# Kernel optimization log

Measured on AMD Instinct MI355X. Metric: run time of the kernel, lower is better.

Reference implementation:

```python
import jax, jax.numpy as jnp
import numpy as np

N = 120000
G = 64  # voxel grid side
HID = 128
INP = 320
CIN = HID + INP  # 448
K = 27


def _build_neighbor_map(rng):
    # unique occupied voxel cells
    cells = rng.choice(G ** 3, size=N, replace=False)
    xs = cells // (G * G)
    ys = (cells // G) % G
    zs = cells % G
    order = np.argsort(cells)
    sk = cells[order]
    offs = np.array([(dx, dy, dz) for dx in (-1, 0, 1) for dy in (-1, 0, 1) for dz in (-1, 0, 1)], dtype=np.int64)
    nx = xs[:, None] + offs[None, :, 0]
    ny = ys[:, None] + offs[None, :, 1]
    nz = zs[:, None] + offs[None, :, 2]
    valid = (nx >= 0) & (nx < G) & (ny >= 0) & (ny < G) & (nz >= 0) & (nz < G)
    nkey = (nx * G + ny) * G + nz
    pos = np.clip(np.searchsorted(sk, nkey), 0, N - 1)
    found = valid & (sk[pos] == nkey)
    return np.where(found, order[pos], -1).astype(np.int32)  # (N, 27)


def setup_inputs() -> dict:
    key = jax.random.key(0)
    ks = jax.random.split(key, 12)
    rng = np.random.default_rng(0)
    nbr = jnp.asarray(_build_neighbor_map(rng))
    s_conv = 1.0 / np.sqrt(K * CIN)
    s_lin = 1.0 / np.sqrt(CIN)
    return {
        "h": jax.random.normal(ks[0], (N, HID), jnp.float32),
        "x": jax.random.normal(ks[1], (N, INP), jnp.float32),
        "nbr": nbr,
        "Wz": jax.random.normal(ks[2], (K, CIN, HID), jnp.float32) * s_conv,
        "Wz_pt": jax.random.normal(ks[3], (CIN, HID), jnp.float32) * s_lin,
        "bz": jnp.zeros((HID,), jnp.float32),
        "Wr": jax.random.normal(ks[4], (K, CIN, HID), jnp.float32) * s_conv,
        "Wr_pt": jax.random.normal(ks[5], (CIN, HID), jnp.float32) * s_lin,
        "br": jnp.zeros((HID,), jnp.float32),
        "Wq": jax.random.normal(ks[6], (K, CIN, HID), jnp.float32) * s_conv,
        "Wq_pt": jax.random.normal(ks[7], (CIN, HID), jnp.float32) * s_lin,
        "bq": jnp.zeros((HID,), jnp.float32),
    }


def _sconv3d(F, nbr, W, W_pt, b_pt):
    # sparse 3x3x3 conv (gather + matmul accumulate over 27 offsets, no conv bias)
    # followed by voxel_to_point (identity here) + point_transforms linear.
    mask = (nbr >= 0)
    idx = jnp.where(mask, nbr, 0)
    out = F @ W_pt + b_pt  # point transform branch
    for k in range(K):  # fixed small kernel-offset loop
        g = F[idx[:, k]] * mask[:, k:k + 1].astype(F.dtype)  # (N, CIN)
        out = out + g @ W[k]
    return out


def reference(h, x, nbr, Wz, Wz_pt, bz, Wr, Wr_pt, br, Wq, Wq_pt, bq):
    hx = jnp.concatenate([h, x], axis=1)  # (N, 448)
    z = jax.nn.sigmoid(_sconv3d(hx, nbr, Wz, Wz_pt, bz))
    r = jax.nn.sigmoid(_sconv3d(hx, nbr, Wr, Wr_pt, br))
    rx = jnp.concatenate([r * h, x], axis=1)
    q = jnp.tanh(_sconv3d(rx, nbr, Wq, Wq_pt, bq))
    return (1.0 - z) * h + z * q
```

## Files before the change

kernel.cpp:

```cpp
#include <hip/hip_runtime.h>

#define NPTS   120000
#define NOFF   28
#define CHUNKS 7

typedef __bf16 bf16;
typedef __bf16 bf16x8 __attribute__((ext_vector_type(8)));
typedef float  f32x4  __attribute__((ext_vector_type(4)));

__global__ void wprep1(const float* __restrict__ Wz, const float* __restrict__ Wzp,
                       const float* __restrict__ Wr, const float* __restrict__ Wrp,
                       bf16* __restrict__ WB1)
{
    int bid  = blockIdx.x;
    int koff = bid / 56;
    int rem  = bid % 56;
    int ch   = rem / 8;
    int kseg = rem % 8;
    int n    = threadIdx.x;
    int cinb = ch * 64 + kseg * 8;
    bf16x8 v;
    if (n < 128) {
        int col = n;
        #pragma unroll
        for (int j = 0; j < 8; ++j) {
            int cin = cinb + j;
            float w = (koff < 27) ? Wz[((long)koff * 448 + cin) * 128 + col]
                                  : Wzp[(long)cin * 128 + col];
            v[j] = (bf16)w;
        }
    } else {
        int col = n - 128;
        #pragma unroll
        for (int j = 0; j < 8; ++j) {
            int cin = cinb + j;
            float w = (koff < 27) ? Wr[((long)koff * 448 + cin) * 128 + col]
                                  : Wrp[(long)cin * 128 + col];
            v[j] = (bf16)w;
        }
    }
    *(bf16x8*)(WB1 + ((long)bid * 256 + n) * 8) = v;
}

__global__ void wprep2(const float* __restrict__ Wq, const float* __restrict__ Wqp,
                       bf16* __restrict__ WB2)
{
    int bid  = blockIdx.x;
    int koff = bid / 56;
    int rem  = bid % 56;
    int ch   = rem / 8;
    int kseg = rem % 8;
    int n    = threadIdx.x;
    int cinb = ch * 64 + kseg * 8;
    bf16x8 v;
    #pragma unroll
    for (int j = 0; j < 8; ++j) {
        int cin = cinb + j;
        float w = (koff < 27) ? Wq[((long)koff * 448 + cin) * 128 + n]
                              : Wqp[(long)cin * 128 + n];
        v[j] = (bf16)w;
    }
    *(bf16x8*)(WB2 + ((long)bid * 128 + n) * 8) = v;
}

__global__ void fprep(const float* __restrict__ h, const float* __restrict__ x,
                      bf16* __restrict__ F1, bf16* __restrict__ F2)
{
    long i = (long)blockIdx.x * blockDim.x + threadIdx.x;
    if (i >= (long)NPTS * 448) return;
    int p = (int)(i / 448);
    int c = (int)(i % 448);
    float v = (c < 128) ? h[(long)p * 128 + c] : x[(long)p * 320 + (c - 128)];
    F1[i] = (bf16)v;
    if (c >= 128) F2[i] = (bf16)v;
}

template<int NCOLS, int GATE>
__global__ __launch_bounds__(NCOLS * 2)
void gconv(const bf16* __restrict__ F, const int* __restrict__ nbr,
           const bf16* __restrict__ WB, const float* __restrict__ b0,
           const float* __restrict__ b1, const float* __restrict__ hbuf,
           float* __restrict__ zbuf, bf16* __restrict__ f2,
           float* __restrict__ out, const bf16* __restrict__ zrow)
{
    constexpr int THREADS = NCOLS * 2;
    constexpr int AP = 1024 / THREADS;
    constexpr int BP = (NCOLS * 8) / THREADS;

    __shared__ __align__(16) bf16 lA[8 * 128 * 8];
    __shared__ __align__(16) bf16 lB[8 * NCOLS * 8];
    __shared__ int lidx[128];

    const int t    = threadIdx.x;
    const int lane = t & 63;
    const int w    = t >> 6;
    const int m0   = (w & 1) * 64;
    const int n0   = (w >> 1) * 64;
    const int base = blockIdx.x * 128;
    const int ar   = t & 127;
    const int aks0 = t >> 7;

    f32x4 acc[4][4];
    #pragma unroll
    for (int i = 0; i < 4; ++i)
        #pragma unroll
        for (int j = 0; j < 4; ++j)
            acc[i][j] = {0.f, 0.f, 0.f, 0.f};

    const bf16x8* lAv = (const bf16x8*)lA;
    const bf16x8* lBv = (const bf16x8*)lB;

    for (int koff = 0; koff < NOFF; ++koff) {
        __syncthreads();
        if (t < 128) {
            int p = base + t;
            int idx = -1;
            if (p < NPTS) idx = (koff == 27) ? p : nbr[(long)p * 27 + koff];
            lidx[t] = idx;
        }
        __syncthreads();
        const int myidx = lidx[ar];
        const bf16* arow = (myidx >= 0) ? (F + (long)myidx * 448) : zrow;

        for (int ch = 0; ch < CHUNKS; ++ch) {
            #pragma unroll
            for (int p = 0; p < AP; ++p) {
                int kseg = aks0 + p * (THREADS / 128);
                __builtin_amdgcn_global_load_lds(
                    (void*)(arow + ch * 64 + kseg * 8),
                    (void*)(lA + ((long)t + (long)p * THREADS) * 8),
                    16, 0, 0);
            }
            const bf16* bsrc = WB + (long)(koff * CHUNKS + ch) * (NCOLS * 64);
            #pragma unroll
            for (int p = 0; p < BP; ++p) {
                __builtin_amdgcn_global_load_lds(
                    (void*)(bsrc + ((long)t + (long)p * THREADS) * 8),
                    (void*)(lB + ((long)t + (long)p * THREADS) * 8),
                    16, 0, 0);
            }
            __syncthreads();
            #pragma unroll
            for (int kk = 0; kk < 2; ++kk) {
                const int aseg = kk * 4 + (lane >> 4);
                bf16x8 af[4], bfr[4];
                #pragma unroll
                for (int mi = 0; mi < 4; ++mi)
                    af[mi] = lAv[aseg * 128 + m0 + mi * 16 + (lane & 15)];
                #pragma unroll
                for (int ni = 0; ni < 4; ++ni)
                    bfr[ni] = lBv[aseg * NCOLS + n0 + ni * 16 + (lane & 15)];
                #pragma unroll
                for (int mi = 0; mi < 4; ++mi)
                    #pragma unroll
                    for (int ni = 0; ni < 4; ++ni)
                        acc[mi][ni] = __builtin_amdgcn_mfma_f32_16x16x32_bf16(
                            af[mi], bfr[ni], acc[mi][ni], 0, 0, 0);
            }
            __syncthreads();
        }
    }

    const int quad = lane >> 4;
    const int lc   = lane & 15;
    #pragma unroll
    for (int mi = 0; mi < 4; ++mi) {
        int rb = m0 + mi * 16 + quad * 4;
        #pragma unroll
        for (int ni = 0; ni < 4; ++ni) {
            int c = n0 + ni * 16 + lc;
            f32x4 v = acc[mi][ni];
            #pragma unroll
            for (int rg = 0; rg < 4; ++rg) {
                int p = base + rb + rg;
                if (p < NPTS) {
                    float pre = v[rg];
                    if constexpr (GATE == 1) {
                        if (c < 128) {
                            float z = 1.f / (1.f + __expf(-(pre + b0[c])));
                            zbuf[(long)p * 128 + c] = z;
                        } else {
                            int cc = c - 128;
                            float r = 1.f / (1.f + __expf(-(pre + b1[cc])));
                            f2[(long)p * 448 + cc] = (bf16)(r * hbuf[(long)p * 128 + cc]);
                        }
                    } else {
                        float q  = tanhf(pre + b0[c]);
                        float z  = zbuf[(long)p * 128 + c];
                        float hv = hbuf[(long)p * 128 + c];
                        out[(long)p * 128 + c] = (1.f - z) * hv + z * q;
                    }
                }
            }
        }
    }
}

extern "C" void kernel_launch(void* const* d_in, const int* in_sizes, int n_in,
                              void* d_out, int out_size, void* d_ws, size_t ws_size,
                              hipStream_t stream)
{
    const float* h   = (const float*)d_in[0];
    const float* x   = (const float*)d_in[1];
    const int*   nbr = (const int*)d_in[2];
    const float* Wz  = (const float*)d_in[3];
    const float* Wzp = (const float*)d_in[4];
    const float* bz  = (const float*)d_in[5];
    const float* Wr  = (const float*)d_in[6];
    const float* Wrp = (const float*)d_in[7];
    const float* br  = (const float*)d_in[8];
    const float* Wq  = (const float*)d_in[9];
    const float* Wqp = (const float*)d_in[10];
    const float* bq  = (const float*)d_in[11];
    float* out = (float*)d_out;

    char* ws = (char*)d_ws;
    bf16* WB1 = (bf16*)ws;  ws += (size_t)1568 * 256 * 8 * 2;
    bf16* WB2 = (bf16*)ws;  ws += (size_t)1568 * 128 * 8 * 2;
    bf16* F1  = (bf16*)ws;  ws += (size_t)NPTS * 448 * 2;
    bf16* F2  = (bf16*)ws;  ws += (size_t)NPTS * 448 * 2;
    bf16* zrow = (bf16*)ws; ws += 1024;
    float* zbuf = out;

    hipMemsetAsync(zrow, 0, 1024, stream);
    wprep1<<<1568, 256, 0, stream>>>(Wz, Wzp, Wr, Wrp, WB1);
    wprep2<<<1568, 128, 0, stream>>>(Wq, Wqp, WB2);
    long total = (long)NPTS * 448;
    fprep<<<(int)((total + 255) / 256), 256, 0, stream>>>(h, x, F1, F2);

    int grid = (NPTS + 127) / 128;
    gconv<256, 1><<<grid, 512, 0, stream>>>(F1, nbr, WB1, bz, br, h, zbuf, F2, nullptr, zrow);
    gconv<128, 2><<<grid, 256, 0, stream>>>(F2, nbr, WB2, bq, nullptr, h, zbuf, nullptr, out, zrow);
}
```

Baseline: 1.752 ms.

## Share x features between stages, vectorize fprep, use 256-row tiles for q conv

The second conv now reads its x channels directly from F1 and only the r*h part from a compact 128-wide F2, so the full 448-wide F2 copy is no longer written. fprep is vectorized to handle eight channels per thread with float4 loads and a bf16x8 store. The q-conv kernel is generalized to a templated row tile and launched with 256 rows and 512 threads, so each weight tile fetched into LDS is reused across twice as many points. In exchange the A-gather in the second stage now reads from two separate buffers, and the larger tile gives fewer blocks for the scheduler.

```diff
diff --git a/kernel.cpp b/kernel.cpp
--- a/kernel.cpp
+++ b/kernel.cpp
@@ -64,41 +64,47 @@
 }
 
 __global__ void fprep(const float* __restrict__ h, const float* __restrict__ x,
-                      bf16* __restrict__ F1, bf16* __restrict__ F2)
-{
-    long i = (long)blockIdx.x * blockDim.x + threadIdx.x;
-    if (i >= (long)NPTS * 448) return;
-    int p = (int)(i / 448);
-    int c = (int)(i % 448);
-    float v = (c < 128) ? h[(long)p * 128 + c] : x[(long)p * 320 + (c - 128)];
-    F1[i] = (bf16)v;
-    if (c >= 128) F2[i] = (bf16)v;
-}
-
-template<int NCOLS, int GATE>
-__global__ __launch_bounds__(NCOLS * 2)
+                      bf16* __restrict__ F1)
+{
+    long g = (long)blockIdx.x * blockDim.x + threadIdx.x;
+    if (g >= (long)NPTS * 56) return;
+    int p = (int)(g / 56);
+    int c = (int)(g % 56) * 8;
+    const float* src = (c < 128) ? h + (long)p * 128 + c
+                                 : x + (long)p * 320 + (c - 128);
+    float4 a = ((const float4*)src)[0];
+    float4 b = ((const float4*)src)[1];
+    bf16x8 v;
+    v[0] = (bf16)a.x; v[1] = (bf16)a.y; v[2] = (bf16)a.z; v[3] = (bf16)a.w;
+    v[4] = (bf16)b.x; v[5] = (bf16)b.y; v[6] = (bf16)b.z; v[7] = (bf16)b.w;
+    *(bf16x8*)(F1 + (long)p * 448 + c) = v;
+}
+
+template<int MROWS, int NCOLS, int GATE>
+__global__ __launch_bounds__(512)
 void gconv(const bf16* __restrict__ F, const int* __restrict__ nbr,
            const bf16* __restrict__ WB, const float* __restrict__ b0,
            const float* __restrict__ b1, const float* __restrict__ hbuf,
            float* __restrict__ zbuf, bf16* __restrict__ f2,
            float* __restrict__ out, const bf16* __restrict__ zrow)
 {
-    constexpr int THREADS = NCOLS * 2;
-    constexpr int AP = 1024 / THREADS;
-    constexpr int BP = (NCOLS * 8) / THREADS;
-
-    __shared__ __align__(16) bf16 lA[8 * 128 * 8];
+    constexpr int THREADS = 512;
+    constexpr int MW = MROWS / 64;
+    constexpr int AP = 8 * MROWS / THREADS;
+    constexpr int BP = 8 * NCOLS / THREADS;
+
+    __shared__ __align__(16) bf16 lA[8 * MROWS * 8];
     __shared__ __align__(16) bf16 lB[8 * NCOLS * 8];
-    __shared__ int lidx[128];
+    __shared__ int lidx[MROWS];
 
     const int t    = threadIdx.x;
     const int lane = t & 63;
     const int w    = t >> 6;
-    const int m0   = (w & 1) * 64;
-    const int n0   = (w >> 1) * 64;
-    const int base = blockIdx.x * 128;
-    const int ar   = t & 127;
-    const int aks0 = t >> 7;
+    const int m0   = (w % MW) * 64;
+    const int n0   = (w / MW) * 64;
+    const int base = blockIdx.x * MROWS;
+    const int ar   = t % MROWS;
+    const int aks0 = t / MROWS;
 
     f32x4 acc[4][4];
     #pragma unroll
@@ -112,7 +118,7 @@
 
     for (int koff = 0; koff < NOFF; ++koff) {
         __syncthreads();
-        if (t < 128) {
+        if (t < MROWS) {
             int p = base + t;
             int idx = -1;
             if (p < NPTS) idx = (koff == 27) ? p : nbr[(long)p * 27 + koff];
@@ -120,14 +126,19 @@
         }
         __syncthreads();
         const int myidx = lidx[ar];
-        const bf16* arow = (myidx >= 0) ? (F + (long)myidx * 448) : zrow;
+        const bf16* row1 = (myidx >= 0) ? (F + (long)myidx * 448) : zrow;
+        const bf16* row2 = row1;
+        if constexpr (GATE == 2)
+            row2 = (myidx >= 0) ? (f2 + (long)myidx * 128) : zrow;
 
         for (int ch = 0; ch < CHUNKS; ++ch) {
+            const bf16* asrc = (GATE == 2 && ch < 2) ? (row2 + ch * 64)
+                                                     : (row1 + ch * 64);
             #pragma unroll
             for (int p = 0; p < AP; ++p) {
-                int kseg = aks0 + p * (THREADS / 128);
+                int kseg = aks0 + p * (THREADS / MROWS);
                 __builtin_amdgcn_global_load_lds(
-                    (void*)(arow + ch * 64 + kseg * 8),
+                    (void*)(asrc + kseg * 8),
                     (void*)(lA + ((long)t + (long)p * THREADS) * 8),
                     16, 0, 0);
             }
@@ -146,7 +157,7 @@
                 bf16x8 af[4], bfr[4];
                 #pragma unroll
                 for (int mi = 0; mi < 4; ++mi)
-                    af[mi] = lAv[aseg * 128 + m0 + mi * 16 + (lane & 15)];
+                    af[mi] = lAv[aseg * MROWS + m0 + mi * 16 + (lane & 15)];
                 #pragma unroll
                 for (int ni = 0; ni < 4; ++ni)
                     bfr[ni] = lBv[aseg * NCOLS + n0 + ni * 16 + (lane & 15)];
@@ -182,7 +193,7 @@
                         } else {
                             int cc = c - 128;
                             float r = 1.f / (1.f + __expf(-(pre + b1[cc])));
-                            f2[(long)p * 448 + cc] = (bf16)(r * hbuf[(long)p * 128 + cc]);
+                            f2[(long)p * 128 + cc] = (bf16)(r * hbuf[(long)p * 128 + cc]);
                         }
                     } else {
                         float q  = tanhf(pre + b0[c]);
@@ -218,17 +229,18 @@
     bf16* WB1 = (bf16*)ws;  ws += (size_t)1568 * 256 * 8 * 2;
     bf16* WB2 = (bf16*)ws;  ws += (size_t)1568 * 128 * 8 * 2;
     bf16* F1  = (bf16*)ws;  ws += (size_t)NPTS * 448 * 2;
-    bf16* F2  = (bf16*)ws;  ws += (size_t)NPTS * 448 * 2;
+    bf16* F2  = (bf16*)ws;  ws += (size_t)NPTS * 128 * 2;
     bf16* zrow = (bf16*)ws; ws += 1024;
     float* zbuf = out;
 
     hipMemsetAsync(zrow, 0, 1024, stream);
     wprep1<<<1568, 256, 0, stream>>>(Wz, Wzp, Wr, Wrp, WB1);
     wprep2<<<1568, 128, 0, stream>>>(Wq, Wqp, WB2);
-    long total = (long)NPTS * 448;
-    fprep<<<(int)((total + 255) / 256), 256, 0, stream>>>(h, x, F1, F2);
-
-    int grid = (NPTS + 127) / 128;
-    gconv<256, 1><<<grid, 512, 0, stream>>>(F1, nbr, WB1, bz, br, h, zbuf, F2, nullptr, zrow);
-    gconv<128, 2><<<grid, 256, 0, stream>>>(F2, nbr, WB2, bq, nullptr, h, zbuf, nullptr, out, zrow);
-}
+    long groups = (long)NPTS * 56;
+    fprep<<<(int)((groups + 255) / 256), 256, 0, stream>>>(h, x, F1);
+
+    gconv<128, 256, 1><<<(NPTS + 127) / 128, 512, 0, stream>>>(
+        F1, nbr, WB1, bz, br, h, zbuf, F2, nullptr, zrow);
+    gconv<256, 128, 2><<<(NPTS + 255) / 256, 512, 0, stream>>>(
+        F1, nbr, WB2, bq, nullptr, h, zbuf, F2, out, zrow);
+}
```

After: 1.543 ms. 11.9% less time.
